# Optimization experiments

Measured on AMD Instinct MI355X. Metric: run time of the kernel, lower is better.

## Reference

```python
import jax, jax.numpy as jnp
import numpy as np

MASK_THRED = 1        # init kwarg mask_thred
TRIPLE_WEIGHT = 1.0   # init kwarg triple_weight (scales gradient of shifted branch)
NEG = -1e30
EPS = 1e-8


def setup_inputs() -> dict:
    key = jax.random.key(0)
    k1, k2 = jax.random.split(key)
    x = jax.random.normal(k1, (2, 128, 96, 96), dtype=jnp.float32)
    mask = jax.random.randint(k2, (96, 96), 0, 2, dtype=jnp.int32)
    return {"x": x, "mask": mask}


def reference(x, mask):
    # x: (B, C, H, W); former = x[:, :C//2], latter = x[:, C//2:]
    B, C, H, W = x.shape
    c2 = C // 2
    hw = H * W

    # shift_sz=1, stride=1, mask_thred=1 -> a location is 'masked' iff mask >= 1
    flag = mask.reshape(hw) >= MASK_THRED  # (hw,) True = inside hole

    former, latter = x[:, :c2], x[:, c2:]

    # similarity path is non-differentiable in the original (hard argmax, detached latter)
    lat = jax.lax.stop_gradient(latter).reshape(B, c2, hw).transpose(0, 2, 1)  # (B, hw, c2)
    # original normalizes only the candidate (non-masked) patches (NCC filters)
    lat_n = lat / jnp.maximum(jnp.linalg.norm(lat, axis=-1, keepdims=True), EPS)

    # cross-correlation of every location against every (normalized) candidate
    sim = jnp.einsum('bic,bjc->bij', lat, lat_n)  # (B, hw, hw)
    # only non-masked locations are valid candidates j
    sim = jnp.where(flag[None, None, :], NEG, sim)
    idx = jnp.argmax(sim, axis=-1)  # (B, hw) nearest non-masked neighbor per location

    # shift: copy the FORMER feature from the matched non-masked location
    fmr = former.reshape(B, c2, hw).transpose(0, 2, 1)  # (B, hw, c2)
    gathered = jnp.take_along_axis(fmr, idx[:, :, None], axis=1)  # (B, hw, c2)

    # triple_weight scales only the gradient of the shifted branch (fwd unchanged)
    tw = jnp.float32(TRIPLE_WEIGHT)
    gathered = gathered * tw + jax.lax.stop_gradient(gathered * (1.0 - tw))

    # shifted features only at masked locations, zero elsewhere
    shift = jnp.where(flag[None, :, None], gathered, jnp.float32(0.0))
    shift = shift.transpose(0, 2, 1).reshape(B, c2, H, W)

    # triple: (former, latter, shifted) -> (B, 3*C//2, H, W)
    return jnp.concatenate([former, latter, shift], axis=1)
```

## Files before the change

kernel.cpp:

```cpp
#include <hip/hip_runtime.h>
#include <math.h>

#define HW 9216
#define NSTRIP 288
#define NCH 12
#define EPSN 1e-8f

typedef _Float16 f16x8  __attribute__((ext_vector_type(8)));
typedef float    f32x16 __attribute__((ext_vector_type(16)));

__global__ __launch_bounds__(256) void prep_kernel(
    const float* __restrict__ x, const int* __restrict__ mask,
    int* __restrict__ ilist, int* __restrict__ jlist, int* __restrict__ counts,
    _Float16* __restrict__ aH, _Float16* __restrict__ aL,
    _Float16* __restrict__ bH, _Float16* __restrict__ bL,
    unsigned long long* __restrict__ amax)
{
    __shared__ unsigned short slot16[HW];
    __shared__ int wsum[4];
    int tid = threadIdx.x;
    int base = tid * 36;
    const int4* mp4 = (const int4*)mask + tid * 9;
    unsigned long long fl = 0ull; int cnt = 0;
#pragma unroll
    for (int k4 = 0; k4 < 9; k4++) {
        int4 m4 = mp4[k4];
        int f0 = (m4.x >= 1), f1 = (m4.y >= 1), f2 = (m4.z >= 1), f3 = (m4.w >= 1);
        fl |= ((unsigned long long)f0 << (k4 * 4)) | ((unsigned long long)f1 << (k4 * 4 + 1)) |
              ((unsigned long long)f2 << (k4 * 4 + 2)) | ((unsigned long long)f3 << (k4 * 4 + 3));
        cnt += f0 + f1 + f2 + f3;
    }
    int lane = tid & 63, wave = tid >> 6;
    int v = cnt;
#pragma unroll
    for (int off = 1; off < 64; off <<= 1) {
        int u = __shfl_up(v, off, 64);
        if (lane >= off) v += u;
    }
    if (lane == 63) wsum[wave] = v;
    __syncthreads();
    int woff = 0;
#pragma unroll
    for (int w = 0; w < 4; w++) if (w < wave) woff += wsum[w];
    int incl = v + woff;
    int excl = incl - cnt;
    int posF = excl, posU = base - excl;
    bool wl = (blockIdx.x == 0);
#pragma unroll
    for (int k = 0; k < 36; k++) {
        int p = base + k;
        if ((fl >> k) & 1ull) { slot16[p] = (unsigned short)(posF | 0x8000); if (wl) ilist[posF] = p; posF++; }
        else                  { slot16[p] = (unsigned short)posU;            if (wl) jlist[posU] = p; posU++; }
    }
    if (wl && tid == 255) { counts[0] = incl; counts[1] = HW - incl; }
    __syncthreads();
    int t = blockIdx.x * 256 + tid;
    int sub = t & 63;
    int q = sub >> 4;
    int pb = ((t >> 6) << 4) | (sub & 15);
    int b = pb / HW, p = pb - b * HW;
    const float* xl = x + (size_t)(b * 128 + 64) * HW + p;
    float vv[16]; float ss = 0.f;
#pragma unroll
    for (int e = 0; e < 16; e++) { float w0 = xl[(size_t)(q * 16 + e) * HW]; vv[e] = w0; ss = fmaf(w0, w0, ss); }
    ss += __shfl_xor(ss, 16, 64);
    ss += __shfl_xor(ss, 32, 64);
    float inv = 1.0f / fmaxf(sqrtf(ss), EPSN);
    if (q == 0) amax[pb] = 0ull;
    unsigned sl = slot16[p];
    int flagged = sl >> 15;
    int slot = sl & 0x7fff;
    float scale = flagged ? 1.0f : inv;
    int tile = slot >> 5, lnp = slot & 31;
    _Float16* dh = flagged ? aH : bH;
    _Float16* dl = flagged ? aL : bL;
#pragma unroll
    for (int h = 0; h < 2; h++) {
        size_t off = ((((size_t)b * NSTRIP + tile) * 4 + q) * 64 + h * 32 + lnp) * 8;
        f16x8 hh, ll;
#pragma unroll
        for (int e = 0; e < 8; e++) {
            float w0 = vv[h * 8 + e] * scale;
            _Float16 hv = (_Float16)w0;
            hh[e] = hv; ll[e] = (_Float16)((w0 - (float)hv) * 2048.0f);
        }
        *(f16x8*)(dh + off) = hh; *(f16x8*)(dl + off) = ll;
    }
}

__device__ __forceinline__ unsigned int ordf(float f) {
    unsigned int u = __float_as_uint(f);
    return (u & 0x80000000u) ? ~u : (u | 0x80000000u);
}

__global__ __launch_bounds__(256, 2) void argmax_kernel(
    const _Float16* __restrict__ aH, const _Float16* __restrict__ aL,
    const _Float16* __restrict__ bH, const _Float16* __restrict__ bL,
    const int* __restrict__ ilist, const int* __restrict__ counts,
    unsigned long long* __restrict__ amax)
{
    int ni = counts[0];
    if (blockIdx.x * 256 >= ni) return;
    int nj = counts[1];
    int njt = (nj + 31) >> 5;
    int tpc = (njt + NCH - 1) / NCH;
    int s = blockIdx.y;
    int jt0 = s * tpc, jt1 = min(jt0 + tpc, njt);
    if (jt0 >= jt1) return;
    int b = blockIdx.z;
    int wave = threadIdx.x >> 6, l = threadIdx.x & 63;
    int base = (blockIdx.x * 4 + wave) * 64;
    int g = l >> 5, ln = l & 31;
    int strip0 = base >> 5;

    __shared__ f16x8 lds[2][8][64];

    const f16x8* apH = (const f16x8*)aH + ((size_t)b * NSTRIP + strip0) * 256 + l;
    const f16x8* apL = (const f16x8*)aL + ((size_t)b * NSTRIP + strip0) * 256 + l;
    f16x8 xh0 = apH[0],   xh1 = apH[64],  xh2 = apH[128], xh3 = apH[192];
    f16x8 xl0 = apL[0],   xl1 = apL[64],  xl2 = apL[128], xl3 = apL[192];
    f16x8 yh0 = apH[256], yh1 = apH[320], yh2 = apH[384], yh3 = apH[448];
    f16x8 yl0 = apL[256], yl1 = apL[320], yl2 = apL[384], yl3 = apL[448];

    int f0 = wave * 2;
    const f16x8* s0 = (const f16x8*)((f0 < 4) ? bH : bL) +
                      (size_t)b * NSTRIP * 256 + (size_t)(f0 & 3) * 64 + l;
    const f16x8* s1 = (const f16x8*)((f0 + 1 < 4) ? bH : bL) +
                      (size_t)b * NSTRIP * 256 + (size_t)((f0 + 1) & 3) * 64 + l;

    {
        f16x8 t0 = s0[(size_t)jt0 * 256];
        f16x8 t1 = s1[(size_t)jt0 * 256];
        lds[0][f0][l] = t0;
        lds[0][f0 + 1][l] = t1;
    }
    __syncthreads();

    float bv0 = -INFINITY, bv1 = -INFINITY;
    int bj0 = -1, bj1 = -1;
    int cur = 0;

    for (int jt = jt0; jt < jt1; ++jt, cur ^= 1) {
        f16x8 n0, n1;
        bool more = (jt + 1 < jt1);
        if (more) {
            n0 = s0[(size_t)(jt + 1) * 256];
            n1 = s1[(size_t)(jt + 1) * 256];
        }
        f16x8 bh0 = lds[cur][0][l], bh1 = lds[cur][1][l];
        f16x8 bh2 = lds[cur][2][l], bh3 = lds[cur][3][l];
        f16x8 bl0 = lds[cur][4][l], bl1 = lds[cur][5][l];
        f16x8 bl2 = lds[cur][6][l], bl3 = lds[cur][7][l];
        f32x16 cH0 = {}, cC0 = {}, cH1 = {}, cC1 = {};
        cH0 = __builtin_amdgcn_mfma_f32_32x32x16_f16(bh0, xh0, cH0, 0, 0, 0);
        cC0 = __builtin_amdgcn_mfma_f32_32x32x16_f16(bh0, xl0, cC0, 0, 0, 0);
        cC0 = __builtin_amdgcn_mfma_f32_32x32x16_f16(bl0, xh0, cC0, 0, 0, 0);
        cH0 = __builtin_amdgcn_mfma_f32_32x32x16_f16(bh1, xh1, cH0, 0, 0, 0);
        cC0 = __builtin_amdgcn_mfma_f32_32x32x16_f16(bh1, xl1, cC0, 0, 0, 0);
        cC0 = __builtin_amdgcn_mfma_f32_32x32x16_f16(bl1, xh1, cC0, 0, 0, 0);
        cH0 = __builtin_amdgcn_mfma_f32_32x32x16_f16(bh2, xh2, cH0, 0, 0, 0);
        cC0 = __builtin_amdgcn_mfma_f32_32x32x16_f16(bh2, xl2, cC0, 0, 0, 0);
        cC0 = __builtin_amdgcn_mfma_f32_32x32x16_f16(bl2, xh2, cC0, 0, 0, 0);
        cH0 = __builtin_amdgcn_mfma_f32_32x32x16_f16(bh3, xh3, cH0, 0, 0, 0);
        cC0 = __builtin_amdgcn_mfma_f32_32x32x16_f16(bh3, xl3, cC0, 0, 0, 0);
        cC0 = __builtin_amdgcn_mfma_f32_32x32x16_f16(bl3, xh3, cC0, 0, 0, 0);
        cH1 = __builtin_amdgcn_mfma_f32_32x32x16_f16(bh0, yh0, cH1, 0, 0, 0);
        cC1 = __builtin_amdgcn_mfma_f32_32x32x16_f16(bh0, yl0, cC1, 0, 0, 0);
        cC1 = __builtin_amdgcn_mfma_f32_32x32x16_f16(bl0, yh0, cC1, 0, 0, 0);
        cH1 = __builtin_amdgcn_mfma_f32_32x32x16_f16(bh1, yh1, cH1, 0, 0, 0);
        cC1 = __builtin_amdgcn_mfma_f32_32x32x16_f16(bh1, yl1, cC1, 0, 0, 0);
        cC1 = __builtin_amdgcn_mfma_f32_32x32x16_f16(bl1, yh1, cC1, 0, 0, 0);
        cH1 = __builtin_amdgcn_mfma_f32_32x32x16_f16(bh2, yh2, cH1, 0, 0, 0);
        cC1 = __builtin_amdgcn_mfma_f32_32x32x16_f16(bh2, yl2, cC1, 0, 0, 0);
        cC1 = __builtin_amdgcn_mfma_f32_32x32x16_f16(bl2, yh2, cC1, 0, 0, 0);
        cH1 = __builtin_amdgcn_mfma_f32_32x32x16_f16(bh3, yh3, cH1, 0, 0, 0);
        cC1 = __builtin_amdgcn_mfma_f32_32x32x16_f16(bh3, yl3, cC1, 0, 0, 0);
        cC1 = __builtin_amdgcn_mfma_f32_32x32x16_f16(bl3, yh3, cC1, 0, 0, 0);
        int jb = jt << 5;
        if (jb + 32 <= nj) {
#pragma unroll
            for (int r = 0; r < 16; ++r) {
                int row = (r & 3) + 8 * (r >> 2) + 4 * g;
                int j = jb + row;
                float v0 = fmaf(cC0[r], 4.8828125e-4f , cH0[r]);
                float v1 = fmaf(cC1[r], 4.8828125e-4f, cH1[r]);
                if (v0 > bv0) { bv0 = v0; bj0 = j; }
                if (v1 > bv1) { bv1 = v1; bj1 = j; }
            }
        } else {
#pragma unroll
            for (int r = 0; r < 16; ++r) {
                int row = (r & 3) + 8 * (r >> 2) + 4 * g;
                int j = jb + row;
                float v0 = fmaf(cC0[r], 4.8828125e-4f, cH0[r]);
                float v1 = fmaf(cC1[r], 4.8828125e-4f, cH1[r]);
                if (j < nj && v0 > bv0) { bv0 = v0; bj0 = j; }
                if (j < nj && v1 > bv1) { bv1 = v1; bj1 = j; }
            }
        }
        if (more) {
            lds[cur ^ 1][f0][l] = n0;
            lds[cur ^ 1][f0 + 1][l] = n1;
        }
        __syncthreads();
    }

    unsigned long long k0 = ((unsigned long long)ordf(bv0) << 32) |
                            (unsigned long long)(~(unsigned int)bj0);
    unsigned long long k1 = ((unsigned long long)ordf(bv1) << 32) |
                            (unsigned long long)(~(unsigned int)bj1);
    unsigned long long o0 = __shfl_xor(k0, 32, 64);
    unsigned long long o1 = __shfl_xor(k1, 32, 64);
    if (o0 > k0) k0 = o0;
    if (o1 > k1) k1 = o1;
    int il0 = base + ln, il1 = base + 32 + ln;
    if (g == 0) {
        if (il0 < ni && (unsigned)(k0 >> 32) > 0x007FFFFFu)
            atomicMax(&amax[(size_t)b * HW + ilist[il0]], k0);
        if (il1 < ni && (unsigned)(k1 >> 32) > 0x007FFFFFu)
            atomicMax(&amax[(size_t)b * HW + ilist[il1]], k1);
    }
}

__global__ void epilogue_kernel(const float4* __restrict__ x4, const float* __restrict__ x,
                                const int* __restrict__ mask,
                                const unsigned long long* __restrict__ amax,
                                const int* __restrict__ jlist, float4* __restrict__ out4) {
    const int q = HW / 4;
    int t = blockIdx.x * blockDim.x + threadIdx.x;
    if (t >= 2 * 192 * q) return;
    int pos4 = t % q;
    int c = (t / q) % 192;
    int b = t / (192 * q);
    if (c < 128) {
        out4[t] = x4[((size_t)b * 128 + c) * q + pos4];
    } else {
        float4 v = make_float4(0.f, 0.f, 0.f, 0.f);
        float* vp = &v.x;
        int pos = pos4 * 4;
        const float* xf = x + (size_t)(b * 128 + (c - 128)) * HW;
#pragma unroll
        for (int k = 0; k < 4; k++) {
            int p = pos + k;
            if (mask[p] >= 1) {
                unsigned long long key = amax[(size_t)b * HW + p];
                int j = 0;
                if (key != 0ull) j = jlist[(int)(~(unsigned int)key)];
                vp[k] = xf[j];
            }
        }
        out4[t] = v;
    }
}

extern "C" void kernel_launch(void* const* d_in, const int* in_sizes, int n_in,
                              void* d_out, int out_size, void* d_ws, size_t ws_size,
                              hipStream_t stream) {
    const float* x = (const float*)d_in[0];
    const int* mask = (const int*)d_in[1];
    float4* out4 = (float4*)d_out;

    char* ws = (char*)d_ws;
    int*   counts = (int*)ws;
    int*   ilist  = (int*)(ws + 128);
    int*   jlist  = (int*)(ws + 36992);
    unsigned long long* amax = (unsigned long long*)(ws + 73856);
    _Float16* aH = (_Float16*)(ws + 221312);
    _Float16* aL = (_Float16*)(ws + 221312 + 1 * 2359296);
    _Float16* bH = (_Float16*)(ws + 221312 + 2 * 2359296);
    _Float16* bL = (_Float16*)(ws + 221312 + 3 * 2359296);

    prep_kernel<<<288, 256, 0, stream>>>(x, mask, ilist, jlist, counts,
                                         aH, aL, bH, bL, amax);
    {
        dim3 grid(NSTRIP / 8, NCH, 2);
        argmax_kernel<<<grid, 256, 0, stream>>>(aH, aL, bH, bL, ilist, counts, amax);
    }
    {
        int n = 2 * 192 * (HW / 4);
        epilogue_kernel<<<(n + 255) / 256, 256, 0, stream>>>((const float4*)x, x, mask,
                                                             amax, jlist, out4);
    }
}
```

Before: 105.5 us.

## Move passthrough copy into prep kernel and raise argmax channel split

The copy of former/latter channels into the output moves out of the epilogue and into 160 extra blocks of the prep kernel, so it runs alongside prep work instead of after the argmax. The epilogue now only produces the shifted channels. NCH also rises from 12 to 18, giving the argmax grid more blocks along the channel split. This adds more atomicMax contention and makes the prep launch larger.

Measured after the change: 97.91 us, median of 2. 7.2% less time.

```diff
diff --git a/kernel.cpp b/kernel.cpp
--- a/kernel.cpp
+++ b/kernel.cpp
@@ -3,22 +3,32 @@
 
 #define HW 9216
 #define NSTRIP 288
-#define NCH 12
+#define NCH 18
+#define NCOPY 160
 #define EPSN 1e-8f
 
 typedef _Float16 f16x8  __attribute__((ext_vector_type(8)));
 typedef float    f32x16 __attribute__((ext_vector_type(16)));
 
 __global__ __launch_bounds__(256) void prep_kernel(
-    const float* __restrict__ x, const int* __restrict__ mask,
+    const float* __restrict__ x, const float4* __restrict__ x4,
+    const int* __restrict__ mask,
     int* __restrict__ ilist, int* __restrict__ jlist, int* __restrict__ counts,
     _Float16* __restrict__ aH, _Float16* __restrict__ aL,
     _Float16* __restrict__ bH, _Float16* __restrict__ bL,
-    unsigned long long* __restrict__ amax)
+    unsigned long long* __restrict__ amax, float4* __restrict__ out4)
 {
     __shared__ unsigned short slot16[HW];
     __shared__ int wsum[4];
     int tid = threadIdx.x;
+    if (blockIdx.x >= 288) {
+        const int N = 128 * (HW / 4);
+        for (int e = (blockIdx.x - 288) * 256 + tid; e < 2 * N; e += NCOPY * 256) {
+            int b = e / N, rem = e - b * N;
+            out4[(size_t)b * 192 * (HW / 4) + rem] = x4[(size_t)b * N + rem];
+        }
+        return;
+    }
     int base = tid * 36;
     const int4* mp4 = (const int4*)mask + tid * 9;
     unsigned long long fl = 0ull; int cnt = 0;
@@ -222,35 +232,31 @@
     }
 }
 
-__global__ void epilogue_kernel(const float4* __restrict__ x4, const float* __restrict__ x,
+__global__ void epilogue_kernel(const float* __restrict__ x,
                                 const int* __restrict__ mask,
                                 const unsigned long long* __restrict__ amax,
                                 const int* __restrict__ jlist, float4* __restrict__ out4) {
     const int q = HW / 4;
     int t = blockIdx.x * blockDim.x + threadIdx.x;
-    if (t >= 2 * 192 * q) return;
+    if (t >= 2 * 64 * q) return;
     int pos4 = t % q;
-    int c = (t / q) % 192;
-    int b = t / (192 * q);
-    if (c < 128) {
-        out4[t] = x4[((size_t)b * 128 + c) * q + pos4];
-    } else {
-        float4 v = make_float4(0.f, 0.f, 0.f, 0.f);
-        float* vp = &v.x;
-        int pos = pos4 * 4;
-        const float* xf = x + (size_t)(b * 128 + (c - 128)) * HW;
-#pragma unroll
-        for (int k = 0; k < 4; k++) {
-            int p = pos + k;
-            if (mask[p] >= 1) {
-                unsigned long long key = amax[(size_t)b * HW + p];
-                int j = 0;
-                if (key != 0ull) j = jlist[(int)(~(unsigned int)key)];
-                vp[k] = xf[j];
-            }
-        }
-        out4[t] = v;
-    }
+    int cs = (t / q) % 64;
+    int b = t / (64 * q);
+    float4 v = make_float4(0.f, 0.f, 0.f, 0.f);
+    float* vp = &v.x;
+    int pos = pos4 * 4;
+    const float* xf = x + (size_t)(b * 128 + cs) * HW;
+#pragma unroll
+    for (int k = 0; k < 4; k++) {
+        int p = pos + k;
+        if (mask[p] >= 1) {
+            unsigned long long key = amax[(size_t)b * HW + p];
+            int j = 0;
+            if (key != 0ull) j = jlist[(int)(~(unsigned int)key)];
+            vp[k] = xf[j];
+        }
+    }
+    out4[((size_t)b * 192 + 128 + cs) * q + pos4] = v;
 }
 
 extern "C" void kernel_launch(void* const* d_in, const int* in_sizes, int n_in,
@@ -270,15 +276,15 @@
     _Float16* bH = (_Float16*)(ws + 221312 + 2 * 2359296);
     _Float16* bL = (_Float16*)(ws + 221312 + 3 * 2359296);
 
-    prep_kernel<<<288, 256, 0, stream>>>(x, mask, ilist, jlist, counts,
-                                         aH, aL, bH, bL, amax);
+    prep_kernel<<<288 + NCOPY, 256, 0, stream>>>(x, (const float4*)x, mask,
+                                                 ilist, jlist, counts,
+                                                 aH, aL, bH, bL, amax, out4);
     {
         dim3 grid(NSTRIP / 8, NCH, 2);
         argmax_kernel<<<grid, 256, 0, stream>>>(aH, aL, bH, bL, ilist, counts, amax);
     }
     {
-        int n = 2 * 192 * (HW / 4);
-        epilogue_kernel<<<(n + 255) / 256, 256, 0, stream>>>((const float4*)x, x, mask,
-                                                             amax, jlist, out4);
-    }
-}
+        int n = 2 * 64 * (HW / 4);
+        epilogue_kernel<<<(n + 255) / 256, 256, 0, stream>>>(x, mask, amax, jlist, out4);
+    }
+}
```
